# Kernel tuning notes

Measured on AMD Instinct MI355X. Metric: run time of the kernel, lower is better.

## Reference

```python
import jax, jax.numpy as jnp
import numpy as np

H = 8      # num_attention_heads
DH = 96    # attention_head_size
LN_EPS = 1e-5


def setup_inputs() -> dict:
    key = jax.random.key(0)
    ks = jax.random.split(key, 12)
    B, S, D = 2, 768, 768
    sc = 0.02
    return {
        "hidden_states": jax.random.normal(ks[0], (B, S, D), jnp.float32),
        "distance_matrix": jax.random.uniform(ks[1], (B, S, S), jnp.float32) * 20.0,
        "angle_matrix": jax.random.uniform(ks[2], (B, S, S), jnp.float32) * np.pi,
        "attention_mask": jnp.ones((B, S), jnp.float32),
        "Wq": jax.random.normal(ks[3], (D, D), jnp.float32) * sc,
        "bq": jnp.zeros((D,), jnp.float32),
        "Wk": jax.random.normal(ks[4], (D, D), jnp.float32) * sc,
        "bk": jnp.zeros((D,), jnp.float32),
        "Wv": jax.random.normal(ks[5], (D, D), jnp.float32) * sc,
        "bv": jnp.zeros((D,), jnp.float32),
        "Wd": jax.random.normal(ks[6], (DH,), jnp.float32) * sc,
        "bd": jnp.zeros((DH,), jnp.float32),
        "Wa": jax.random.normal(ks[7], (DH,), jnp.float32) * sc,
        "ba": jnp.zeros((DH,), jnp.float32),
        "Wo": jax.random.normal(ks[8], (D, D), jnp.float32) * sc,
        "bo": jnp.zeros((D,), jnp.float32),
        "ln_g": jnp.ones((D,), jnp.float32),
        "ln_b": jnp.zeros((D,), jnp.float32),
    }


def _heads(x, B, S):
    # [B,S,D] -> [B,H,S,DH]
    return x.reshape(B, S, H, DH).transpose(0, 2, 1, 3)


def reference(hidden_states, distance_matrix, angle_matrix, attention_mask,
              Wq, bq, Wk, bk, Wv, bv, Wd, bd, Wa, ba, Wo, bo, ln_g, ln_b):
    B, S, D = hidden_states.shape
    q = _heads(hidden_states @ Wq.T + bq, B, S)   # [B,H,S,DH]
    k = _heads(hidden_states @ Wk.T + bk, B, S)
    v = _heads(hidden_states @ Wv.T + bv, B, S)

    scores = jnp.einsum('bhid,bhjd->bhij', q, k) / jnp.sqrt(jnp.float32(DH))

    # distance / angle relative-position biases: emb[b,i,j,:] = dist[b,i,j]*Wd + bd
    dist_emb = distance_matrix[..., None] * Wd + bd   # [B,S,S,DH]
    scores = scores + jnp.einsum('bhid,bijd->bhij', q, dist_emb)
    ang_emb = angle_matrix[..., None] * Wa + ba       # [B,S,S,DH]
    scores = scores + jnp.einsum('bhid,bijd->bhij', q, ang_emb)

    # key mask, broadcast over heads and query positions
    scores = scores + (1.0 - attention_mask)[:, None, None, :] * -10000.0

    probs = jax.nn.softmax(scores, axis=-1)           # [B,H,S,S]
    ctx = jnp.einsum('bhij,bhjd->bhid', probs, v)
    ctx = ctx.transpose(0, 2, 1, 3).reshape(B, S, D)  # [B,S,D]

    out = ctx @ Wo.T + bo
    x = out + hidden_states
    mu = jnp.mean(x, axis=-1, keepdims=True)
    var = jnp.var(x, axis=-1, keepdims=True)
    out = (x - mu) * jax.lax.rsqrt(var + LN_EPS) * ln_g + ln_b
    return out, probs
```

## Files before the change

kernel.cpp:

```cpp
#include <hip/hip_runtime.h>
#include <stdint.h>

#define B_  2
#define S_  768
#define D_  768
#define H_  8
#define DH_ 96

typedef unsigned short ushort_t;
typedef __bf16 bf16x8 __attribute__((ext_vector_type(8)));
typedef float  f32x4  __attribute__((ext_vector_type(4)));

__device__ inline ushort_t f2bf(float f) {
    union { float f; unsigned int u; } v; v.f = f;
    unsigned int u = v.u;
    unsigned int r = u + 0x7fffu + ((u >> 16) & 1u);
    return (ushort_t)(r >> 16);
}
__device__ inline float bf2f(ushort_t u) {
    union { unsigned int i; float f; } c; c.i = ((unsigned int)u) << 16;
    return c.f;
}

__device__ inline void glds16(const void* gp, void* lp) {
    auto g = reinterpret_cast<const __attribute__((address_space(1))) uint32_t*>(
        reinterpret_cast<uintptr_t>(gp));
    auto l = reinterpret_cast<__attribute__((address_space(3))) uint32_t*>(
        reinterpret_cast<uintptr_t>(lp));
    __builtin_amdgcn_global_load_lds(g, l, 16, 0, 0);
}

__global__ __launch_bounds__(256) void k_convert(
        const float* __restrict__ X, const float* __restrict__ Wq,
        const float* __restrict__ Wk, const float* __restrict__ Wv,
        const float* __restrict__ Wo,
        ushort_t* __restrict__ Xb, ushort_t* __restrict__ Wb) {
    const int NX4 = (B_ * S_ * D_) / 4;
    const int NW4 = (D_ * D_) / 4;
    int i = blockIdx.x * blockDim.x + threadIdx.x;
    float4 v;
    ushort_t* dst;
    if (i < NX4) {
        v = ((const float4*)X)[i];
        dst = Xb + i * 4;
    } else {
        int wi = i - NX4;
        int sel = wi / NW4;
        int off = wi - sel * NW4;
        const float* src = (sel == 0) ? Wq : (sel == 1) ? Wk : (sel == 2) ? Wv : Wo;
        v = ((const float4*)src)[off];
        dst = Wb + wi * 4;
    }
    ushort4 o;
    o.x = f2bf(v.x); o.y = f2bf(v.y); o.z = f2bf(v.z); o.w = f2bf(v.w);
    *(ushort4*)dst = o;
}

__device__ inline void gemm64_glds(
        const ushort_t* __restrict__ A, int lda,
        const ushort_t* __restrict__ Bt, int ldb,
        int K, int m0, int n0,
        ushort_t* As, ushort_t* Bs, f32x4 acc[2][2]) {
    const int tid  = threadIdx.x;
    const int lane = tid & 63, wave = tid >> 6;
    const int wm = (wave >> 1) * 32, wn = (wave & 1) * 32;
    const int fr = lane & 15, fk = (lane >> 4) * 8;
    const int sr = wave * 16 + (lane >> 2);
    const int sc = (lane & 3) * 8;
    const ushort_t* Ap = A  + (size_t)(m0 + sr) * lda + sc;
    const ushort_t* Bp = Bt + (size_t)(n0 + sr) * ldb + sc;
    ushort_t* AsW = As + wave * 512;
    ushort_t* BsW = Bs + wave * 512;
    for (int kt = 0; kt < K; kt += 32) {
        if (kt) __syncthreads();
        glds16(Ap + kt, AsW);
        glds16(Bp + kt, BsW);
        __syncthreads();
        bf16x8 a0 = *(const bf16x8*)&As[(wm      + fr) * 32 + fk];
        bf16x8 a1 = *(const bf16x8*)&As[(wm + 16 + fr) * 32 + fk];
        bf16x8 b0 = *(const bf16x8*)&Bs[(wn      + fr) * 32 + fk];
        bf16x8 b1 = *(const bf16x8*)&Bs[(wn + 16 + fr) * 32 + fk];
        acc[0][0] = __builtin_amdgcn_mfma_f32_16x16x32_bf16(a0, b0, acc[0][0], 0, 0, 0);
        acc[0][1] = __builtin_amdgcn_mfma_f32_16x16x32_bf16(a0, b1, acc[0][1], 0, 0, 0);
        acc[1][0] = __builtin_amdgcn_mfma_f32_16x16x32_bf16(a1, b0, acc[1][0], 0, 0, 0);
        acc[1][1] = __builtin_amdgcn_mfma_f32_16x16x32_bf16(a1, b1, acc[1][1], 0, 0, 0);
    }
}

__global__ __launch_bounds__(256) void k_qkv(
        const ushort_t* __restrict__ Xb, const ushort_t* __restrict__ Wb,
        const float* __restrict__ bq, const float* __restrict__ bk,
        const float* __restrict__ bv,
        ushort_t* __restrict__ Qb, ushort_t* __restrict__ Kb,
        ushort_t* __restrict__ Vtb) {
    __shared__ __align__(16) ushort_t As[64 * 32];
    __shared__ __align__(16) ushort_t Bs[64 * 32];
    f32x4 acc[2][2];
    #pragma unroll
    for (int i = 0; i < 2; i++)
        #pragma unroll
        for (int j = 0; j < 2; j++) acc[i][j] = (f32x4){0.f, 0.f, 0.f, 0.f};
    const int m0 = blockIdx.y * 64, n0 = blockIdx.x * 64;
    gemm64_glds(Xb, D_, Wb, D_, D_, m0, n0, As, Bs, acc);
    const int lane = threadIdx.x & 63, wave = threadIdx.x >> 6;
    const int wm = (wave >> 1) * 32, wn = (wave & 1) * 32;
    #pragma unroll
    for (int ni = 0; ni < 2; ni++) {
        int gcol = n0 + wn + ni * 16 + (lane & 15);
        int g = gcol / D_, d768 = gcol - g * D_;
        int h = d768 / DH_, d = d768 - h * DH_;
        float bias = (g == 0 ? bq : (g == 1 ? bk : bv))[d768];
        #pragma unroll
        for (int mi = 0; mi < 2; mi++) {
            #pragma unroll
            for (int r = 0; r < 4; r++) {
                int grow = m0 + wm + mi * 16 + (lane >> 4) * 4 + r;
                int b = grow / S_, s = grow - b * S_;
                ushort_t ob = f2bf(acc[mi][ni][r] + bias);
                int bh = b * H_ + h;
                if (g == 0)      Qb[((size_t)bh * S_ + s) * DH_ + d] = ob;
                else if (g == 1) Kb[((size_t)bh * S_ + s) * DH_ + d] = ob;
                else             Vtb[((size_t)bh * DH_ + d) * S_ + s] = ob;
            }
        }
    }
}

__global__ __launch_bounds__(256) void k_qcoef(
        const ushort_t* __restrict__ Qb,
        const float* __restrict__ Wd, const float* __restrict__ bd,
        const float* __restrict__ Wa, const float* __restrict__ ba,
        float* __restrict__ qcoef) {
    const int wave = threadIdx.x >> 6, lane = threadIdx.x & 63;
    const int row = blockIdx.x * 4 + wave;
    const ushort_t* q = Qb + (size_t)row * DH_;
    float e0 = bf2f(q[lane]);
    float c0 = e0 * Wd[lane];
    float c1 = e0 * Wa[lane];
    float c2 = e0 * (bd[lane] + ba[lane]);
    if (lane < 32) {
        int d = 64 + lane;
        float e1 = bf2f(q[d]);
        c0 += e1 * Wd[d];
        c1 += e1 * Wa[d];
        c2 += e1 * (bd[d] + ba[d]);
    }
    #pragma unroll
    for (int o = 32; o > 0; o >>= 1) {
        c0 += __shfl_down(c0, o);
        c1 += __shfl_down(c1, o);
        c2 += __shfl_down(c2, o);
    }
    if (lane == 0) {
        qcoef[row * 3 + 0] = c0;
        qcoef[row * 3 + 1] = c1;
        qcoef[row * 3 + 2] = c2;
    }
}

#define L1B 29696
__global__ __launch_bounds__(256) void k_flash(
        const ushort_t* __restrict__ Qb, const ushort_t* __restrict__ Kb,
        const ushort_t* __restrict__ Vtb, const float* __restrict__ qcoef,
        const float* __restrict__ distm, const float* __restrict__ angm,
        const float* __restrict__ mask,
        float* __restrict__ probs, ushort_t* __restrict__ Ctxb) {
    __shared__ __align__(16) char sm[2 * L1B + 640];
    float* mstat = (float*)(sm + 2 * L1B);
    float* lstat = (float*)(sm + 2 * L1B + 256);
    float* linv  = (float*)(sm + 2 * L1B + 512);
    const int idx = blockIdx.x;
    const int h = idx / 48, rem = idx - h * 48;
    const int b = rem / 24, r0 = (rem - b * 24) * 32;
    const int bh = b * H_ + h;
    const int tid = threadIdx.x, lane = tid & 63, w = tid >> 6;
    const int frn = lane & 15, fko = (lane >> 4) * 8, frg4 = (lane >> 4) * 4;
    const int rg = w & 1, cp = w >> 1;
    const ushort_t* Qbh = Qb + (size_t)bh * S_ * DH_;
    const ushort_t* Kbh = Kb + (size_t)bh * S_ * DH_;
    const ushort_t* Vbh = Vtb + (size_t)bh * DH_ * S_;

    bf16x8 aq[3];
    {
        const ushort_t* qp = Qbh + (size_t)(r0 + rg * 16 + frn) * DH_ + fko;
        aq[0] = *(const bf16x8*)qp;
        aq[1] = *(const bf16x8*)(qp + 32);
        aq[2] = *(const bf16x8*)(qp + 64);
    }
    float qc0[4], qc1[4], qc2[4];
    #pragma unroll
    for (int r = 0; r < 4; r++) {
        const float* qp = qcoef + ((size_t)bh * S_ + r0 + rg * 16 + frg4 + r) * 3;
        qc0[r] = qp[0]; qc1[r] = qp[1]; qc2[r] = qp[2];
    }
    const float isq = 0.10206207261596577f;

    f32x4 acc[24];
    #pragma unroll
    for (int c = 0; c < 12; ++c) {
        char* bufc = sm + (c & 1) * L1B;
        ushort_t* Ks = (ushort_t*)bufc;
        float* Dd = (float*)(bufc + 12288);
        float* Da = (float*)(bufc + 20992);
        #pragma unroll
        for (int k = 0; k < 3; ++k) {
            int i = tid + 256 * k;
            int row = i / 12, cc = (i - row * 12) * 8;
            *(uint4*)(Ks + row * 96 + cc) =
                *(const uint4*)(Kbh + (size_t)(c * 64 + row) * DH_ + cc);
        }
        #pragma unroll
        for (int k = 0; k < 2; ++k) {
            int i = tid + 256 * k;
            int row = i >> 4, c4 = (i & 15) * 4;
            size_t src = ((size_t)b * S_ + r0 + row) * S_ + c * 64 + c4;
            *(float4*)(Dd + row * 68 + c4) = *(const float4*)(distm + src);
            *(float4*)(Da + row * 68 + c4) = *(const float4*)(angm + src);
        }
        __syncthreads();
        #pragma unroll
        for (int tt = 0; tt < 2; ++tt) {
            const ushort_t* kp = Ks + (cp * 32 + tt * 16 + frn) * 96 + fko;
            f32x4 ca = (f32x4){0.f, 0.f, 0.f, 0.f};
            ca = __builtin_amdgcn_mfma_f32_16x16x32_bf16(aq[0], *(const bf16x8*)kp, ca, 0, 0, 0);
            ca = __builtin_amdgcn_mfma_f32_16x16x32_bf16(aq[1], *(const bf16x8*)(kp + 32), ca, 0, 0, 0);
            ca = __builtin_amdgcn_mfma_f32_16x16x32_bf16(aq[2], *(const bf16x8*)(kp + 64), ca, 0, 0, 0);
            int jl = cp * 32 + tt * 16 + frn;
            float mb = (1.0f - mask[b * S_ + c * 64 + jl]) * -10000.0f;
            #pragma unroll
            for (int r = 0; r < 4; ++r) {
                int rl = rg * 16 + frg4 + r;
                acc[c * 2 + tt][r] = ca[r] * isq + Dd[rl * 68 + jl] * qc0[r]
                                   + Da[rl * 68 + jl] * qc1[r] + qc2[r] + mb;
            }
        }
    }
    float mx[4] = {-1e30f, -1e30f, -1e30f, -1e30f};
    #pragma unroll
    for (int t = 0; t < 24; t++)
        #pragma unroll
        for (int r = 0; r < 4; r++) mx[r] = fmaxf(mx[r], acc[t][r]);
    #pragma unroll
    for (int o = 1; o < 16; o <<= 1)
        #pragma unroll
        for (int r = 0; r < 4; r++) mx[r] = fmaxf(mx[r], __shfl_xor(mx[r], o));
    if (frn == 0)
        #pragma unroll
        for (int r = 0; r < 4; r++) mstat[cp * 32 + rg * 16 + frg4 + r] = mx[r];
    __syncthreads();
    float mf[4], sum[4] = {0.f, 0.f, 0.f, 0.f};
    #pragma unroll
    for (int r = 0; r < 4; r++) {
        int rl = rg * 16 + frg4 + r;
        mf[r] = fmaxf(mstat[rl], mstat[32 + rl]);
    }
    #pragma unroll
    for (int t = 0; t < 24; t++)
        #pragma unroll
        for (int r = 0; r < 4; r++) {
            float e = __expf(acc[t][r] - mf[r]);
            acc[t][r] = e;
            sum[r] += e;
        }
    #pragma unroll
    for (int o = 1; o < 16; o <<= 1)
        #pragma unroll
        for (int r = 0; r < 4; r++) sum[r] += __shfl_xor(sum[r], o);
    if (frn == 0)
        #pragma unroll
        for (int r = 0; r < 4; r++) lstat[cp * 32 + rg * 16 + frg4 + r] = sum[r];
    __syncthreads();
    float inv[4];
    #pragma unroll
    for (int r = 0; r < 4; r++) {
        int rl = rg * 16 + frg4 + r;
        inv[r] = 1.0f / (lstat[rl] + lstat[32 + rl]);
        if (cp == 0 && frn == 0) linv[rl] = inv[r];
    }
    __syncthreads();
    f32x4 accO[3];
    #pragma unroll
    for (int i = 0; i < 3; i++) accO[i] = (f32x4){0.f, 0.f, 0.f, 0.f};
    const int prow = tid >> 3, pc8 = (tid & 7) * 4;
    float* pout = probs + ((size_t)bh * S_ + r0 + prow) * S_;
    const int vrow = tid >> 2, vcv = (tid & 3) * 8;
    const int vrow2 = (tid + 256) >> 2, vcv2 = ((tid + 256) & 3) * 8;
    #pragma unroll
    for (int s = 0; s < 24; ++s) {
        ushort_t* Vs = (ushort_t*)(sm + (s & 1) * 7680);
        ushort_t* Ps = (ushort_t*)(sm + 15360 + (s & 1) * 2560);
        *(uint4*)(Vs + vrow * 40 + vcv) =
            *(const uint4*)(Vbh + (size_t)vrow * S_ + s * 32 + vcv);
        if (tid + 256 < 384)
            *(uint4*)(Vs + vrow2 * 40 + vcv2) =
                *(const uint4*)(Vbh + (size_t)vrow2 * S_ + s * 32 + vcv2);
        if (cp == (s & 1)) {
            #pragma unroll
            for (int tt = 0; tt < 2; ++tt)
                #pragma unroll
                for (int r = 0; r < 4; ++r)
                    Ps[(rg * 16 + frg4 + r) * 40 + tt * 16 + frn] =
                        f2bf(acc[(s & ~1) + tt][r]);
        }
        __syncthreads();
        {
            float iv = linv[prow];
            float4 p4;
            p4.x = bf2f(Ps[prow * 40 + pc8 + 0]) * iv;
            p4.y = bf2f(Ps[prow * 40 + pc8 + 1]) * iv;
            p4.z = bf2f(Ps[prow * 40 + pc8 + 2]) * iv;
            p4.w = bf2f(Ps[prow * 40 + pc8 + 3]) * iv;
            *(float4*)(pout + s * 32 + pc8) = p4;
        }
        bf16x8 a = *(const bf16x8*)&Ps[(rg * 16 + frn) * 40 + fko];
        #pragma unroll
        for (int nt = 0; nt < 3; ++nt) {
            bf16x8 v = *(const bf16x8*)&Vs[(cp * 48 + nt * 16 + frn) * 40 + fko];
            accO[nt] = __builtin_amdgcn_mfma_f32_16x16x32_bf16(a, v, accO[nt], 0, 0, 0);
        }
    }
    #pragma unroll
    for (int nt = 0; nt < 3; ++nt) {
        int col = h * DH_ + cp * 48 + nt * 16 + frn;
        #pragma unroll
        for (int r = 0; r < 4; ++r) {
            int row = r0 + rg * 16 + frg4 + r;
            Ctxb[((size_t)(b * S_ + row)) * D_ + col] = f2bf(accO[nt][r] * inv[r]);
        }
    }
}

__global__ __launch_bounds__(256) void k_out(
        const ushort_t* __restrict__ Ctxb, const ushort_t* __restrict__ Wob,
        const float* __restrict__ bo, const float* __restrict__ hidden,
        float* __restrict__ xbuf) {
    __shared__ __align__(16) ushort_t As[64 * 32];
    __shared__ __align__(16) ushort_t Bs[64 * 32];
    f32x4 acc[2][2];
    #pragma unroll
    for (int i = 0; i < 2; i++)
        #pragma unroll
        for (int j = 0; j < 2; j++) acc[i][j] = (f32x4){0.f, 0.f, 0.f, 0.f};
    const int m0 = blockIdx.y * 64, n0 = blockIdx.x * 64;
    gemm64_glds(Ctxb, D_, Wob, D_, D_, m0, n0, As, Bs, acc);
    const int lane = threadIdx.x & 63, wave = threadIdx.x >> 6;
    const int wm = (wave >> 1) * 32, wn = (wave & 1) * 32;
    #pragma unroll
    for (int ni = 0; ni < 2; ni++) {
        int gcol = n0 + wn + ni * 16 + (lane & 15);
        float bias = bo[gcol];
        #pragma unroll
        for (int mi = 0; mi < 2; mi++) {
            #pragma unroll
            for (int r = 0; r < 4; r++) {
                int grow = m0 + wm + mi * 16 + (lane >> 4) * 4 + r;
                xbuf[(size_t)grow * D_ + gcol] =
                    acc[mi][ni][r] + bias + hidden[(size_t)grow * D_ + gcol];
            }
        }
    }
}

__global__ __launch_bounds__(256) void k_ln(
        const float* __restrict__ xbuf, const float* __restrict__ g,
        const float* __restrict__ bb, float* __restrict__ out) {
    const float* x = xbuf + (size_t)blockIdx.x * D_;
    const int t = threadIdx.x;
    float a0 = x[t], a1 = x[t + 256], a2 = x[t + 512];
    float s = a0 + a1 + a2;
    float ss = a0 * a0 + a1 * a1 + a2 * a2;
    __shared__ float r1[4], r2[4];
    #pragma unroll
    for (int o = 32; o > 0; o >>= 1) { s += __shfl_down(s, o); ss += __shfl_down(ss, o); }
    if ((t & 63) == 0) { r1[t >> 6] = s; r2[t >> 6] = ss; }
    __syncthreads();
    float ts = r1[0] + r1[1] + r1[2] + r1[3];
    float tss = r2[0] + r2[1] + r2[2] + r2[3];
    float mu = ts * (1.0f / D_);
    float var = tss * (1.0f / D_) - mu * mu;
    float rstd = rsqrtf(var + 1e-5f);
    float* o = out + (size_t)blockIdx.x * D_;
    o[t]       = (a0 - mu) * rstd * g[t]       + bb[t];
    o[t + 256] = (a1 - mu) * rstd * g[t + 256] + bb[t + 256];
    o[t + 512] = (a2 - mu) * rstd * g[t + 512] + bb[t + 512];
}

extern "C" void kernel_launch(void* const* d_in, const int* in_sizes, int n_in,
                              void* d_out, int out_size, void* d_ws, size_t ws_size,
                              hipStream_t stream) {
    const float* X     = (const float*)d_in[0];
    const float* distm = (const float*)d_in[1];
    const float* angm  = (const float*)d_in[2];
    const float* mask  = (const float*)d_in[3];
    const float* Wq    = (const float*)d_in[4];
    const float* bq    = (const float*)d_in[5];
    const float* Wk    = (const float*)d_in[6];
    const float* bk    = (const float*)d_in[7];
    const float* Wv    = (const float*)d_in[8];
    const float* bv    = (const float*)d_in[9];
    const float* Wd    = (const float*)d_in[10];
    const float* bd    = (const float*)d_in[11];
    const float* Wa    = (const float*)d_in[12];
    const float* ba    = (const float*)d_in[13];
    const float* Wo    = (const float*)d_in[14];
    const float* bo    = (const float*)d_in[15];
    const float* ln_g  = (const float*)d_in[16];
    const float* ln_b  = (const float*)d_in[17];

    float* outp  = (float*)d_out;
    float* probs = (float*)d_out + (size_t)B_ * S_ * D_;

    char* ws = (char*)d_ws;
    ushort_t* Xb    = (ushort_t*)(ws + 0);
    ushort_t* Wb    = (ushort_t*)(ws + 2359296);
    ushort_t* Qb    = (ushort_t*)(ws + 7077888);
    ushort_t* Kb    = (ushort_t*)(ws + 9437184);
    ushort_t* Vtb   = (ushort_t*)(ws + 11796480);
    ushort_t* Ctxb  = (ushort_t*)(ws + 14155776);
    float*    qcoef = (float*)   (ws + 16515072);
    float*    xbuf  = (float*)   (ws + 16662528);

    k_convert<<<3456, 256, 0, stream>>>(X, Wq, Wk, Wv, Wo, Xb, Wb);
    k_qkv<<<dim3(36, 24), 256, 0, stream>>>(Xb, Wb, bq, bk, bv, Qb, Kb, Vtb);
    k_qcoef<<<3072, 256, 0, stream>>>(Qb, Wd, bd, Wa, ba, qcoef);
    k_flash<<<384, 256, 0, stream>>>(Qb, Kb, Vtb, qcoef, distm, angm, mask, probs, Ctxb);
    k_out<<<dim3(12, 24), 256, 0, stream>>>(Ctxb, Wb + (size_t)2304 * 768, bo, X, xbuf);
    k_ln<<<1536, 256, 0, stream>>>(xbuf, ln_g, ln_b, outp);
}
```

Baseline: 180.8 us.

## Fuse fp32-to-bf16 conversion into GEMMs and software-pipeline flash tile loads

Removes the separate conversion kernel. The QKV and output GEMMs now read fp32 X and weights directly, converting to bf16 while staging into double-buffered LDS with register prefetch of the next K tile. The flash kernel prefetches the next K/distance/angle tile and the next V tile into registers during compute, and precomputes the mask bias into LDS. This trades more fp32 global traffic per GEMM tile and extra register pressure for one fewer launch and better latency hiding.

```diff
diff --git a/kernel.cpp b/kernel.cpp
--- a/kernel.cpp
+++ b/kernel.cpp
@@ -10,6 +10,7 @@
 typedef unsigned short ushort_t;
 typedef __bf16 bf16x8 __attribute__((ext_vector_type(8)));
 typedef float  f32x4  __attribute__((ext_vector_type(4)));
+typedef unsigned short u16x8 __attribute__((ext_vector_type(8)));
 
 __device__ inline ushort_t f2bf(float f) {
     union { float f; unsigned int u; } v; v.f = f;
@@ -21,100 +22,84 @@
     union { unsigned int i; float f; } c; c.i = ((unsigned int)u) << 16;
     return c.f;
 }
-
-__device__ inline void glds16(const void* gp, void* lp) {
-    auto g = reinterpret_cast<const __attribute__((address_space(1))) uint32_t*>(
-        reinterpret_cast<uintptr_t>(gp));
-    auto l = reinterpret_cast<__attribute__((address_space(3))) uint32_t*>(
-        reinterpret_cast<uintptr_t>(lp));
-    __builtin_amdgcn_global_load_lds(g, l, 16, 0, 0);
-}
-
-__global__ __launch_bounds__(256) void k_convert(
-        const float* __restrict__ X, const float* __restrict__ Wq,
-        const float* __restrict__ Wk, const float* __restrict__ Wv,
-        const float* __restrict__ Wo,
-        ushort_t* __restrict__ Xb, ushort_t* __restrict__ Wb) {
-    const int NX4 = (B_ * S_ * D_) / 4;
-    const int NW4 = (D_ * D_) / 4;
-    int i = blockIdx.x * blockDim.x + threadIdx.x;
-    float4 v;
-    ushort_t* dst;
-    if (i < NX4) {
-        v = ((const float4*)X)[i];
-        dst = Xb + i * 4;
-    } else {
-        int wi = i - NX4;
-        int sel = wi / NW4;
-        int off = wi - sel * NW4;
-        const float* src = (sel == 0) ? Wq : (sel == 1) ? Wk : (sel == 2) ? Wv : Wo;
-        v = ((const float4*)src)[off];
-        dst = Wb + wi * 4;
-    }
-    ushort4 o;
-    o.x = f2bf(v.x); o.y = f2bf(v.y); o.z = f2bf(v.z); o.w = f2bf(v.w);
-    *(ushort4*)dst = o;
-}
-
-__device__ inline void gemm64_glds(
-        const ushort_t* __restrict__ A, int lda,
-        const ushort_t* __restrict__ Bt, int ldb,
-        int K, int m0, int n0,
-        ushort_t* As, ushort_t* Bs, f32x4 acc[2][2]) {
-    const int tid  = threadIdx.x;
-    const int lane = tid & 63, wave = tid >> 6;
+__device__ inline void cvt8st(ushort_t* dst, float4 a, float4 b) {
+    u16x8 o;
+    o[0] = f2bf(a.x); o[1] = f2bf(a.y); o[2] = f2bf(a.z); o[3] = f2bf(a.w);
+    o[4] = f2bf(b.x); o[5] = f2bf(b.y); o[6] = f2bf(b.z); o[7] = f2bf(b.w);
+    *(u16x8*)dst = o;
+}
+
+__global__ __launch_bounds__(256) void k_qkv(
+        const float* __restrict__ X,
+        const float* __restrict__ Wq, const float* __restrict__ Wk,
+        const float* __restrict__ Wv,
+        const float* __restrict__ bq, const float* __restrict__ bk,
+        const float* __restrict__ bv,
+        ushort_t* __restrict__ Qb, ushort_t* __restrict__ Kb,
+        ushort_t* __restrict__ Vtb) {
+    __shared__ __align__(16) ushort_t As[2][64 * 32];
+    __shared__ __align__(16) ushort_t Bs[2][64 * 32];
+    const int tid = threadIdx.x, lane = tid & 63, wave = tid >> 6;
     const int wm = (wave >> 1) * 32, wn = (wave & 1) * 32;
-    const int fr = lane & 15, fk = (lane >> 4) * 8;
-    const int sr = wave * 16 + (lane >> 2);
-    const int sc = (lane & 3) * 8;
-    const ushort_t* Ap = A  + (size_t)(m0 + sr) * lda + sc;
-    const ushort_t* Bp = Bt + (size_t)(n0 + sr) * ldb + sc;
-    ushort_t* AsW = As + wave * 512;
-    ushort_t* BsW = Bs + wave * 512;
-    for (int kt = 0; kt < K; kt += 32) {
-        if (kt) __syncthreads();
-        glds16(Ap + kt, AsW);
-        glds16(Bp + kt, BsW);
-        __syncthreads();
-        bf16x8 a0 = *(const bf16x8*)&As[(wm      + fr) * 32 + fk];
-        bf16x8 a1 = *(const bf16x8*)&As[(wm + 16 + fr) * 32 + fk];
-        bf16x8 b0 = *(const bf16x8*)&Bs[(wn      + fr) * 32 + fk];
-        bf16x8 b1 = *(const bf16x8*)&Bs[(wn + 16 + fr) * 32 + fk];
+    const int fr = lane & 15, fk = (lane >> 4) * 8, frg4 = (lane >> 4) * 4;
+    const int m0 = blockIdx.y * 64, n0 = blockIdx.x * 64;
+    const int g = n0 / D_, nb = n0 - g * D_;
+    const float* W      = (g == 0) ? Wq : (g == 1) ? Wk : Wv;
+    const float* bias_p = (g == 0) ? bq : (g == 1) ? bk : bv;
+    const int sr = wave * 16 + (lane >> 2), sc = (lane & 3) * 8;
+    const float* Ap = X + (size_t)(m0 + sr) * D_ + sc;
+    const float* Bp = W + (size_t)(nb + sr) * D_ + sc;
+    ushort_t* Asd = &As[0][sr * 32 + sc];
+    ushort_t* Bsd = &Bs[0][sr * 32 + sc];
+    const int bufstride = 64 * 32;
+
+    float4 a0r, a1r, b0r, b1r;
+    a0r = *(const float4*)(Ap);     a1r = *(const float4*)(Ap + 4);
+    b0r = *(const float4*)(Bp);     b1r = *(const float4*)(Bp + 4);
+    cvt8st(Asd, a0r, a1r);
+    cvt8st(Bsd, b0r, b1r);
+    __syncthreads();
+
+    f32x4 acc[2][2];
+    #pragma unroll
+    for (int i = 0; i < 2; i++)
+        #pragma unroll
+        for (int j = 0; j < 2; j++) acc[i][j] = (f32x4){0.f, 0.f, 0.f, 0.f};
+
+    for (int c = 0; c < 24; ++c) {
+        if (c < 23) {
+            const float* Apn = Ap + (c + 1) * 32;
+            const float* Bpn = Bp + (c + 1) * 32;
+            a0r = *(const float4*)(Apn);     a1r = *(const float4*)(Apn + 4);
+            b0r = *(const float4*)(Bpn);     b1r = *(const float4*)(Bpn + 4);
+        }
+        const ushort_t* Ab = As[c & 1];
+        const ushort_t* Bb = Bs[c & 1];
+        bf16x8 a0 = *(const bf16x8*)&Ab[(wm      + fr) * 32 + fk];
+        bf16x8 a1 = *(const bf16x8*)&Ab[(wm + 16 + fr) * 32 + fk];
+        bf16x8 b0 = *(const bf16x8*)&Bb[(wn      + fr) * 32 + fk];
+        bf16x8 b1 = *(const bf16x8*)&Bb[(wn + 16 + fr) * 32 + fk];
         acc[0][0] = __builtin_amdgcn_mfma_f32_16x16x32_bf16(a0, b0, acc[0][0], 0, 0, 0);
         acc[0][1] = __builtin_amdgcn_mfma_f32_16x16x32_bf16(a0, b1, acc[0][1], 0, 0, 0);
         acc[1][0] = __builtin_amdgcn_mfma_f32_16x16x32_bf16(a1, b0, acc[1][0], 0, 0, 0);
         acc[1][1] = __builtin_amdgcn_mfma_f32_16x16x32_bf16(a1, b1, acc[1][1], 0, 0, 0);
-    }
-}
-
-__global__ __launch_bounds__(256) void k_qkv(
-        const ushort_t* __restrict__ Xb, const ushort_t* __restrict__ Wb,
-        const float* __restrict__ bq, const float* __restrict__ bk,
-        const float* __restrict__ bv,
-        ushort_t* __restrict__ Qb, ushort_t* __restrict__ Kb,
-        ushort_t* __restrict__ Vtb) {
-    __shared__ __align__(16) ushort_t As[64 * 32];
-    __shared__ __align__(16) ushort_t Bs[64 * 32];
-    f32x4 acc[2][2];
-    #pragma unroll
-    for (int i = 0; i < 2; i++)
-        #pragma unroll
-        for (int j = 0; j < 2; j++) acc[i][j] = (f32x4){0.f, 0.f, 0.f, 0.f};
-    const int m0 = blockIdx.y * 64, n0 = blockIdx.x * 64;
-    gemm64_glds(Xb, D_, Wb, D_, D_, m0, n0, As, Bs, acc);
-    const int lane = threadIdx.x & 63, wave = threadIdx.x >> 6;
-    const int wm = (wave >> 1) * 32, wn = (wave & 1) * 32;
+        if (c < 23) {
+            int nb2 = (c + 1) & 1;
+            cvt8st(Asd + nb2 * bufstride, a0r, a1r);
+            cvt8st(Bsd + nb2 * bufstride, b0r, b1r);
+        }
+        __syncthreads();
+    }
     #pragma unroll
     for (int ni = 0; ni < 2; ni++) {
-        int gcol = n0 + wn + ni * 16 + (lane & 15);
-        int g = gcol / D_, d768 = gcol - g * D_;
+        int d768 = nb + wn + ni * 16 + fr;
         int h = d768 / DH_, d = d768 - h * DH_;
-        float bias = (g == 0 ? bq : (g == 1 ? bk : bv))[d768];
+        float bias = bias_p[d768];
         #pragma unroll
         for (int mi = 0; mi < 2; mi++) {
             #pragma unroll
             for (int r = 0; r < 4; r++) {
-                int grow = m0 + wm + mi * 16 + (lane >> 4) * 4 + r;
+                int grow = m0 + wm + mi * 16 + frg4 + r;
                 int b = grow / S_, s = grow - b * S_;
                 ushort_t ob = f2bf(acc[mi][ni][r] + bias);
                 int bh = b * H_ + h;
@@ -165,10 +150,11 @@
         const float* __restrict__ distm, const float* __restrict__ angm,
         const float* __restrict__ mask,
         float* __restrict__ probs, ushort_t* __restrict__ Ctxb) {
-    __shared__ __align__(16) char sm[2 * L1B + 640];
+    __shared__ __align__(16) char sm[2 * L1B + 640 + 3072];
     float* mstat = (float*)(sm + 2 * L1B);
     float* lstat = (float*)(sm + 2 * L1B + 256);
     float* linv  = (float*)(sm + 2 * L1B + 512);
+    float* Ms    = (float*)(sm + 2 * L1B + 640);
     const int idx = blockIdx.x;
     const int h = idx / 48, rem = idx - h * 48;
     const int b = rem / 24, r0 = (rem - b * 24) * 32;
@@ -180,6 +166,10 @@
     const ushort_t* Kbh = Kb + (size_t)bh * S_ * DH_;
     const ushort_t* Vbh = Vtb + (size_t)bh * DH_ * S_;
 
+    Ms[tid]       = (1.0f - mask[b * S_ + tid])       * -10000.0f;
+    Ms[tid + 256] = (1.0f - mask[b * S_ + tid + 256]) * -10000.0f;
+    Ms[tid + 512] = (1.0f - mask[b * S_ + tid + 512]) * -10000.0f;
+
     bf16x8 aq[3];
     {
         const ushort_t* qp = Qbh + (size_t)(r0 + rg * 16 + frn) * DH_ + fko;
@@ -195,29 +185,52 @@
     }
     const float isq = 0.10206207261596577f;
 
+    const int krow = tid / 12,        kcc = (tid - krow * 12) * 8;
+    const int krow1 = (tid + 256) / 12, kcc1 = ((tid + 256) % 12) * 8;
+    const int krow2 = (tid + 512) / 12, kcc2 = ((tid + 512) % 12) * 8;
+    const int drow = tid >> 4,  dc4 = (tid & 15) * 4;
+    const int drow1 = (tid + 256) >> 4, dc41 = ((tid + 256) & 15) * 4;
+
+    uint4 kr0, kr1, kr2; float4 dr0, dr1, ar0, ar1;
+    {
+        kr0 = *(const uint4*)(Kbh + (size_t)krow  * DH_ + kcc);
+        kr1 = *(const uint4*)(Kbh + (size_t)krow1 * DH_ + kcc1);
+        kr2 = *(const uint4*)(Kbh + (size_t)krow2 * DH_ + kcc2);
+        size_t s0 = ((size_t)b * S_ + r0 + drow)  * S_ + dc4;
+        size_t s1 = ((size_t)b * S_ + r0 + drow1) * S_ + dc41;
+        dr0 = *(const float4*)(distm + s0);  dr1 = *(const float4*)(distm + s1);
+        ar0 = *(const float4*)(angm  + s0);  ar1 = *(const float4*)(angm  + s1);
+    }
+    {
+        ushort_t* Ks = (ushort_t*)sm;
+        float* Dd = (float*)(sm + 12288);
+        float* Da = (float*)(sm + 20992);
+        *(uint4*)(Ks + krow * 96 + kcc)   = kr0;
+        *(uint4*)(Ks + krow1 * 96 + kcc1) = kr1;
+        *(uint4*)(Ks + krow2 * 96 + kcc2) = kr2;
+        *(float4*)(Dd + drow * 68 + dc4)   = dr0;
+        *(float4*)(Dd + drow1 * 68 + dc41) = dr1;
+        *(float4*)(Da + drow * 68 + dc4)   = ar0;
+        *(float4*)(Da + drow1 * 68 + dc41) = ar1;
+    }
+    __syncthreads();
+
     f32x4 acc[24];
-    #pragma unroll
     for (int c = 0; c < 12; ++c) {
+        if (c < 11) {
+            const ushort_t* kb = Kbh + (size_t)(c + 1) * 64 * DH_;
+            kr0 = *(const uint4*)(kb + (size_t)krow  * DH_ + kcc);
+            kr1 = *(const uint4*)(kb + (size_t)krow1 * DH_ + kcc1);
+            kr2 = *(const uint4*)(kb + (size_t)krow2 * DH_ + kcc2);
+            size_t s0 = ((size_t)b * S_ + r0 + drow)  * S_ + (c + 1) * 64 + dc4;
+            size_t s1 = ((size_t)b * S_ + r0 + drow1) * S_ + (c + 1) * 64 + dc41;
+            dr0 = *(const float4*)(distm + s0);  dr1 = *(const float4*)(distm + s1);
+            ar0 = *(const float4*)(angm  + s0);  ar1 = *(const float4*)(angm  + s1);
+        }
         char* bufc = sm + (c & 1) * L1B;
-        ushort_t* Ks = (ushort_t*)bufc;
-        float* Dd = (float*)(bufc + 12288);
-        float* Da = (float*)(bufc + 20992);
-        #pragma unroll
-        for (int k = 0; k < 3; ++k) {
-            int i = tid + 256 * k;
-            int row = i / 12, cc = (i - row * 12) * 8;
-            *(uint4*)(Ks + row * 96 + cc) =
-                *(const uint4*)(Kbh + (size_t)(c * 64 + row) * DH_ + cc);
-        }
-        #pragma unroll
-        for (int k = 0; k < 2; ++k) {
-            int i = tid + 256 * k;
-            int row = i >> 4, c4 = (i & 15) * 4;
-            size_t src = ((size_t)b * S_ + r0 + row) * S_ + c * 64 + c4;
-            *(float4*)(Dd + row * 68 + c4) = *(const float4*)(distm + src);
-            *(float4*)(Da + row * 68 + c4) = *(const float4*)(angm + src);
-        }
-        __syncthreads();
+        const ushort_t* Ks = (const ushort_t*)bufc;
+        const float* Dd = (const float*)(bufc + 12288);
+        const float* Da = (const float*)(bufc + 20992);
         #pragma unroll
         for (int tt = 0; tt < 2; ++tt) {
             const ushort_t* kp = Ks + (cp * 32 + tt * 16 + frn) * 96 + fko;
@@ -226,7 +239,7 @@
             ca = __builtin_amdgcn_mfma_f32_16x16x32_bf16(aq[1], *(const bf16x8*)(kp + 32), ca, 0, 0, 0);
             ca = __builtin_amdgcn_mfma_f32_16x16x32_bf16(aq[2], *(const bf16x8*)(kp + 64), ca, 0, 0, 0);
             int jl = cp * 32 + tt * 16 + frn;
-            float mb = (1.0f - mask[b * S_ + c * 64 + jl]) * -10000.0f;
+            float mb = Ms[c * 64 + jl];
             #pragma unroll
             for (int r = 0; r < 4; ++r) {
                 int rl = rg * 16 + frg4 + r;
@@ -234,7 +247,22 @@
                                    + Da[rl * 68 + jl] * qc1[r] + qc2[r] + mb;
             }
         }
-    }
+        if (c < 11) {
+            char* bufn = sm + ((c + 1) & 1) * L1B;
+            ushort_t* Ksn = (ushort_t*)bufn;
+            float* Ddn = (float*)(bufn + 12288);
+            float* Dan = (float*)(bufn + 20992);
+            *(uint4*)(Ksn + krow * 96 + kcc)   = kr0;
+            *(uint4*)(Ksn + krow1 * 96 + kcc1) = kr1;
+            *(uint4*)(Ksn + krow2 * 96 + kcc2) = kr2;
+            *(float4*)(Ddn + drow * 68 + dc4)   = dr0;
+            *(float4*)(Ddn + drow1 * 68 + dc41) = dr1;
+            *(float4*)(Dan + drow * 68 + dc4)   = ar0;
+            *(float4*)(Dan + drow1 * 68 + dc41) = ar1;
+        }
+        __syncthreads();
+    }
+
     float mx[4] = {-1e30f, -1e30f, -1e30f, -1e30f};
     #pragma unroll
     for (int t = 0; t < 24; t++)
@@ -278,6 +306,7 @@
         if (cp == 0 && frn == 0) linv[rl] = inv[r];
     }
     __syncthreads();
+
     f32x4 accO[3];
     #pragma unroll
     for (int i = 0; i < 3; i++) accO[i] = (f32x4){0.f, 0.f, 0.f, 0.f};
@@ -285,24 +314,31 @@
     float* pout = probs + ((size_t)bh * S_ + r0 + prow) * S_;
     const int vrow = tid >> 2, vcv = (tid & 3) * 8;
     const int vrow2 = (tid + 256) >> 2, vcv2 = ((tid + 256) & 3) * 8;
-    #pragma unroll
-    for (int s = 0; s < 24; ++s) {
-        ushort_t* Vs = (ushort_t*)(sm + (s & 1) * 7680);
-        ushort_t* Ps = (ushort_t*)(sm + 15360 + (s & 1) * 2560);
-        *(uint4*)(Vs + vrow * 40 + vcv) =
-            *(const uint4*)(Vbh + (size_t)vrow * S_ + s * 32 + vcv);
-        if (tid + 256 < 384)
-            *(uint4*)(Vs + vrow2 * 40 + vcv2) =
-                *(const uint4*)(Vbh + (size_t)vrow2 * S_ + s * 32 + vcv2);
-        if (cp == (s & 1)) {
+    const bool hasv2 = (tid < 128);
+    uint4 vr0, vr1;
+    vr0 = *(const uint4*)(Vbh + (size_t)vrow * S_ + vcv);
+    if (hasv2) vr1 = *(const uint4*)(Vbh + (size_t)vrow2 * S_ + vcv2);
+    {
+        ushort_t* Vs = (ushort_t*)(sm);
+        ushort_t* Ps = (ushort_t*)(sm + 15360);
+        *(uint4*)(Vs + vrow * 40 + vcv) = vr0;
+        if (hasv2) *(uint4*)(Vs + vrow2 * 40 + vcv2) = vr1;
+        if (cp == 0) {
             #pragma unroll
             for (int tt = 0; tt < 2; ++tt)
                 #pragma unroll
                 for (int r = 0; r < 4; ++r)
-                    Ps[(rg * 16 + frg4 + r) * 40 + tt * 16 + frn] =
-                        f2bf(acc[(s & ~1) + tt][r]);
-        }
-        __syncthreads();
+                    Ps[(rg * 16 + frg4 + r) * 40 + tt * 16 + frn] = f2bf(acc[tt][r]);
+        }
+    }
+    __syncthreads();
+    for (int s = 0; s < 24; ++s) {
+        if (s < 23) {
+            vr0 = *(const uint4*)(Vbh + (size_t)vrow * S_ + (s + 1) * 32 + vcv);
+            if (hasv2) vr1 = *(const uint4*)(Vbh + (size_t)vrow2 * S_ + (s + 1) * 32 + vcv2);
+        }
+        const ushort_t* Vs = (const ushort_t*)(sm + (s & 1) * 7680);
+        const ushort_t* Ps = (const ushort_t*)(sm + 15360 + (s & 1) * 2560);
         {
             float iv = linv[prow];
             float4 p4;
@@ -318,6 +354,21 @@
             bf16x8 v = *(const bf16x8*)&Vs[(cp * 48 + nt * 16 + frn) * 40 + fko];
             accO[nt] = __builtin_amdgcn_mfma_f32_16x16x32_bf16(a, v, accO[nt], 0, 0, 0);
         }
+        if (s < 23) {
+            ushort_t* Vsn = (ushort_t*)(sm + ((s + 1) & 1) * 7680);
+            ushort_t* Psn = (ushort_t*)(sm + 15360 + ((s + 1) & 1) * 2560);
+            *(uint4*)(Vsn + vrow * 40 + vcv) = vr0;
+            if (hasv2) *(uint4*)(Vsn + vrow2 * 40 + vcv2) = vr1;
+            if (cp == ((s + 1) & 1)) {
+                #pragma unroll
+                for (int tt = 0; tt < 2; ++tt)
+                    #pragma unroll
+                    for (int r = 0; r < 4; ++r)
+                        Psn[(rg * 16 + frg4 + r) * 40 + tt * 16 + frn] =
+                            f2bf(acc[((s + 1) & ~1) + tt][r]);
+            }
+        }
+        __syncthreads();
     }
     #pragma unroll
     for (int nt = 0; nt < 3; ++nt) {
@@ -331,29 +382,67 @@
 }
 
 __global__ __launch_bounds__(256) void k_out(
-        const ushort_t* __restrict__ Ctxb, const ushort_t* __restrict__ Wob,
+        const ushort_t* __restrict__ Ctxb, const float* __restrict__ Wo,
         const float* __restrict__ bo, const float* __restrict__ hidden,
         float* __restrict__ xbuf) {
-    __shared__ __align__(16) ushort_t As[64 * 32];
-    __shared__ __align__(16) ushort_t Bs[64 * 32];
+    __shared__ __align__(16) ushort_t As[2][64 * 32];
+    __shared__ __align__(16) ushort_t Bs[2][64 * 32];
+    const int tid = threadIdx.x, lane = tid & 63, wave = tid >> 6;
+    const int wm = (wave >> 1) * 32, wn = (wave & 1) * 32;
+    const int fr = lane & 15, fk = (lane >> 4) * 8, frg4 = (lane >> 4) * 4;
+    const int m0 = blockIdx.y * 64, n0 = blockIdx.x * 64;
+    const int sr = wave * 16 + (lane >> 2), sc = (lane & 3) * 8;
+    const ushort_t* Ap = Ctxb + (size_t)(m0 + sr) * D_ + sc;
+    const float*    Bp = Wo   + (size_t)(n0 + sr) * D_ + sc;
+    const int bufstride = 64 * 32;
+    ushort_t* Asd = &As[0][sr * 32 + sc];
+    ushort_t* Bsd = &Bs[0][sr * 32 + sc];
+
+    uint4 arr; float4 b0r, b1r;
+    arr = *(const uint4*)(Ap);
+    b0r = *(const float4*)(Bp);  b1r = *(const float4*)(Bp + 4);
+    *(uint4*)Asd = arr;
+    cvt8st(Bsd, b0r, b1r);
+    __syncthreads();
+
     f32x4 acc[2][2];
     #pragma unroll
     for (int i = 0; i < 2; i++)
         #pragma unroll
         for (int j = 0; j < 2; j++) acc[i][j] = (f32x4){0.f, 0.f, 0.f, 0.f};
-    const int m0 = blockIdx.y * 64, n0 = blockIdx.x * 64;
-    gemm64_glds(Ctxb, D_, Wob, D_, D_, m0, n0, As, Bs, acc);
-    const int lane = threadIdx.x & 63, wave = threadIdx.x >> 6;
-    const int wm = (wave >> 1) * 32, wn = (wave & 1) * 32;
+
+    for (int c = 0; c < 24; ++c) {
+        if (c < 23) {
+            arr = *(const uint4*)(Ap + (c + 1) * 32);
+            b0r = *(const float4*)(Bp + (c + 1) * 32);
+            b1r = *(const float4*)(Bp + (c + 1) * 32 + 4);
+        }
+        const ushort_t* Ab = As[c & 1];
+        const ushort_t* Bb = Bs[c & 1];
+        bf16x8 a0 = *(const bf16x8*)&Ab[(wm      + fr) * 32 + fk];
+        bf16x8 a1 = *(const bf16x8*)&Ab[(wm + 16 + fr) * 32 + fk];
+        bf16x8 b0 = *(const bf16x8*)&Bb[(wn      + fr) * 32 + fk];
+        bf16x8 b1 = *(const bf16x8*)&Bb[(wn + 16 + fr) * 32 + fk];
+        acc[0][0] = __builtin_amdgcn_mfma_f32_16x16x32_bf16(a0, b0, acc[0][0], 0, 0, 0);
+        acc[0][1] = __builtin_amdgcn_mfma_f32_16x16x32_bf16(a0, b1, acc[0][1], 0, 0, 0);
+        acc[1][0] = __builtin_amdgcn_mfma_f32_16x16x32_bf16(a1, b0, acc[1][0], 0, 0, 0);
+        acc[1][1] = __builtin_amdgcn_mfma_f32_16x16x32_bf16(a1, b1, acc[1][1], 0, 0, 0);
+        if (c < 23) {
+            int nb2 = (c + 1) & 1;
+            *(uint4*)(Asd + nb2 * bufstride) = arr;
+            cvt8st(Bsd + nb2 * bufstride, b0r, b1r);
+        }
+        __syncthreads();
+    }
     #pragma unroll
     for (int ni = 0; ni < 2; ni++) {
-        int gcol = n0 + wn + ni * 16 + (lane & 15);
+        int gcol = n0 + wn + ni * 16 + fr;
         float bias = bo[gcol];
         #pragma unroll
         for (int mi = 0; mi < 2; mi++) {
             #pragma unroll
             for (int r = 0; r < 4; r++) {
-                int grow = m0 + wm + mi * 16 + (lane >> 4) * 4 + r;
+                int grow = m0 + wm + mi * 16 + frg4 + r;
                 xbuf[(size_t)grow * D_ + gcol] =
                     acc[mi][ni][r] + bias + hidden[(size_t)grow * D_ + gcol];
             }
@@ -411,19 +500,16 @@
     float* probs = (float*)d_out + (size_t)B_ * S_ * D_;
 
     char* ws = (char*)d_ws;
-    ushort_t* Xb    = (ushort_t*)(ws + 0);
-    ushort_t* Wb    = (ushort_t*)(ws + 2359296);
-    ushort_t* Qb    = (ushort_t*)(ws + 7077888);
-    ushort_t* Kb    = (ushort_t*)(ws + 9437184);
-    ushort_t* Vtb   = (ushort_t*)(ws + 11796480);
-    ushort_t* Ctxb  = (ushort_t*)(ws + 14155776);
-    float*    qcoef = (float*)   (ws + 16515072);
-    float*    xbuf  = (float*)   (ws + 16662528);
-
-    k_convert<<<3456, 256, 0, stream>>>(X, Wq, Wk, Wv, Wo, Xb, Wb);
-    k_qkv<<<dim3(36, 24), 256, 0, stream>>>(Xb, Wb, bq, bk, bv, Qb, Kb, Vtb);
+    ushort_t* Qb    = (ushort_t*)(ws + 0);
+    ushort_t* Kb    = (ushort_t*)(ws + 2359296);
+    ushort_t* Vtb   = (ushort_t*)(ws + 4718592);
+    ushort_t* Ctxb  = (ushort_t*)(ws + 7077888);
+    float*    qcoef = (float*)   (ws + 9437184);
+    float*    xbuf  = (float*)   (ws + 9584640);
+
+    k_qkv<<<dim3(36, 24), 256, 0, stream>>>(X, Wq, Wk, Wv, bq, bk, bv, Qb, Kb, Vtb);
     k_qcoef<<<3072, 256, 0, stream>>>(Qb, Wd, bd, Wa, ba, qcoef);
     k_flash<<<384, 256, 0, stream>>>(Qb, Kb, Vtb, qcoef, distm, angm, mask, probs, Ctxb);
-    k_out<<<dim3(12, 24), 256, 0, stream>>>(Ctxb, Wb + (size_t)2304 * 768, bo, X, xbuf);
+    k_out<<<dim3(12, 24), 256, 0, stream>>>(Ctxb, Wo, bo, X, xbuf);
     k_ln<<<1536, 256, 0, stream>>>(xbuf, ln_g, ln_b, outp);
 }
```

Measured after the change: 194.3 us. +7.4%, slower.
